# Optimization experiments

Measured on AMD Instinct MI355X. Metric: run time of the kernel, lower is better.

Reference implementation:

```python
import jax, jax.numpy as jnp
import numpy as np

NUM_HEADS = 16
LN_EPS = 1e-6

B, S, D, INTER = 16, 729, 1152, 4304


def setup_inputs() -> dict:
    key = jax.random.key(0)
    ks = jax.random.split(key, 8)
    std = 0.02
    return {
        "hidden_state": jax.random.normal(ks[0], (B, S, D), jnp.float32),
        "probe": jax.random.normal(ks[1], (1, 1, D), jnp.float32),
        "in_proj_weight": jax.random.normal(ks[2], (3 * D, D), jnp.float32) * std,
        "in_proj_bias": jax.random.normal(ks[3], (3 * D,), jnp.float32) * std,
        "ln_weight": jnp.ones((D,), jnp.float32),
        "ln_bias": jnp.zeros((D,), jnp.float32),
        "fc1_w": jax.random.normal(ks[4], (INTER, D), jnp.float32) * std,
        "fc1_b": jnp.zeros((INTER,), jnp.float32),
        "fc2_w": jax.random.normal(ks[5], (D, INTER), jnp.float32) * std,
        "fc2_b": jnp.zeros((D,), jnp.float32),
    }


def reference(hidden_state, probe, in_proj_weight, in_proj_bias,
              ln_weight, ln_bias, fc1_w, fc1_b, fc2_w, fc2_b):
    b, s, d = hidden_state.shape
    h = NUM_HEADS
    hd = d // h
    Wq, Wk, Wv = in_proj_weight[:d], in_proj_weight[d:2 * d], in_proj_weight[2 * d:]
    bq, bk, bv = in_proj_bias[:d], in_proj_bias[d:2 * d], in_proj_bias[2 * d:]

    # Projections (F.linear: x @ W.T + b)
    q = jnp.broadcast_to(probe, (b, 1, d)) @ Wq.T + bq          # [b,1,d]
    k = hidden_state @ Wk.T + bk                                 # [b,s,d]
    v = hidden_state @ Wv.T + bv                                 # [b,s,d] (this is the 'value' the head keeps)

    # Single-query attention scores per head; embed splits to (h, hd)
    qh = q.reshape(b, h, hd) / jnp.sqrt(jnp.asarray(hd, q.dtype))  # [b,h,hd]
    kh = k.reshape(b, s, h, hd)                                    # [b,s,h,hd]
    scores = jnp.einsum('bhd,bshd->bhs', qh, kh)                   # [b,h,s]
    attn_weights = jax.nn.softmax(scores, axis=-1)                 # [b,h,s]
    # NOTE: original module computes attn_output + out_proj but discards them.

    # Residual MLP on value
    mu = jnp.mean(v, axis=-1, keepdims=True)
    var = jnp.var(v, axis=-1, keepdims=True)
    vn = (v - mu) / jnp.sqrt(var + LN_EPS) * ln_weight + ln_bias
    mlp = jax.nn.gelu(vn @ fc1_w.T + fc1_b, approximate=True) @ fc2_w.T + fc2_b
    out = v + mlp                                                  # [b,s,d]
    return out, attn_weights
```

## Files before the change

### kernel.cpp

```cpp
#include <hip/hip_runtime.h>
#include <hip/hip_bf16.h>

typedef __bf16 bf16;
typedef __bf16 bf16x4 __attribute__((ext_vector_type(4)));
typedef __bf16 bf16x8 __attribute__((ext_vector_type(8)));
typedef float f32x4 __attribute__((ext_vector_type(4)));

#define NB 16
#define NS 729
#define ND 1152
#define NDP 1280
#define NH 16
#define NHD 72
#define NI 4304
#define NM (NB*NS)
#define MP 11776
#define NIP 4352
#define NQ (ND/4)
#define OUT0 ((size_t)NM*(size_t)ND)
#define LNEPS 1e-6f

#define GLOAD16(gp, lp) __builtin_amdgcn_global_load_lds( \
    (const __attribute__((address_space(1))) void*)(gp),  \
    (__attribute__((address_space(3))) void*)(lp), 16, 0, 0)

static __device__ __forceinline__ void nt_store_f32(float v, float* p) {
  __builtin_nontemporal_store(v, p);
}

__global__ __launch_bounds__(256) void k_conv_w(const float* __restrict__ src,
                                                bf16* __restrict__ dst,
                                                int sR, int sC, int dR, int dC) {
  int idx = blockIdx.x * 256 + threadIdx.x;
  int rowlen = dC >> 2;
  int r = idx / rowlen;
  int c = (idx - r * rowlen) * 4;
  if (r >= dR) return;
  bf16x4 o;
  if (r < sR && c + 4 <= sC) {
    float4 v = *(const float4*)(&src[(size_t)r * sC + c]);
    o[0] = (bf16)v.x; o[1] = (bf16)v.y; o[2] = (bf16)v.z; o[3] = (bf16)v.w;
  } else {
    o[0] = (bf16)0.f; o[1] = (bf16)0.f; o[2] = (bf16)0.f; o[3] = (bf16)0.f;
  }
  *(bf16x4*)(&dst[(size_t)r * dC + c]) = o;
}

__global__ __launch_bounds__(256) void k_q(const float* __restrict__ Wq,
                                           const float* __restrict__ probe,
                                           const float* __restrict__ bq,
                                           float* __restrict__ q) {
  int d = blockIdx.x;
  const float* wrow = Wq + (size_t)d * ND;
  float s = 0.f;
  for (int e = threadIdx.x; e < ND; e += 256) s += wrow[e] * probe[e];
  for (int o = 32; o; o >>= 1) s += __shfl_down(s, o, 64);
  __shared__ float sm[4];
  if ((threadIdx.x & 63) == 0) sm[threadIdx.x >> 6] = s;
  __syncthreads();
  if (threadIdx.x == 0) q[d] = sm[0] + sm[1] + sm[2] + sm[3] + bq[d];
}

__global__ __launch_bounds__(256) void k_qk(const float* __restrict__ Wk,
                                            const float* __restrict__ bk,
                                            const float* __restrict__ q,
                                            float* __restrict__ qk,
                                            float* __restrict__ qb) {
  int idx = blockIdx.x * 256 + threadIdx.x;
  if (idx >= NH * ND) return;
  int h = idx / ND, e = idx - h * ND;
  const float scale = 0.11785113019775793f;
  float s = 0.f;
  for (int j = 0; j < NHD; ++j)
    s += q[h * NHD + j] * Wk[(size_t)(h * NHD + j) * ND + e];
  qk[idx] = s * scale;
  if (e == 0) {
    float sb = 0.f;
    for (int j = 0; j < NHD; ++j) sb += q[h * NHD + j] * bk[h * NHD + j];
    qb[h] = sb * scale;
  }
}

__global__ __launch_bounds__(256) void k_scores(const float* __restrict__ hs,
                                                const float* __restrict__ qk,
                                                const float* __restrict__ qb,
                                                float* __restrict__ attn,
                                                bf16* __restrict__ hsb) {
  int p = blockIdx.x;
  int t = threadIdx.x;
  bf16x4* orow4 = (bf16x4*)(hsb + (size_t)p * ND);
  if (p >= NM) {
    bf16x4 z;
    z[0] = (bf16)0.f; z[1] = (bf16)0.f; z[2] = (bf16)0.f; z[3] = (bf16)0.f;
    for (int i = t; i < NQ; i += 256) orow4[i] = z;
    return;
  }
  const f32x4* row4 = (const f32x4*)(hs + (size_t)p * ND);
  const f32x4* qk4 = (const f32x4*)qk;
  float acc[NH];
#pragma unroll
  for (int h = 0; h < NH; ++h) acc[h] = 0.f;
  for (int i = t; i < NQ; i += 256) {
    f32x4 x = __builtin_nontemporal_load(&row4[i]);
    bf16x4 o;
    o[0] = (bf16)x[0]; o[1] = (bf16)x[1]; o[2] = (bf16)x[2]; o[3] = (bf16)x[3];
    orow4[i] = o;
#pragma unroll
    for (int h = 0; h < NH; ++h) {
      f32x4 wv = qk4[h * NQ + i];
      acc[h] = fmaf(x[0], wv[0],
               fmaf(x[1], wv[1], fmaf(x[2], wv[2], fmaf(x[3], wv[3], acc[h]))));
    }
  }
  __shared__ float part[NH][257];
#pragma unroll
  for (int h = 0; h < NH; ++h) part[h][t] = acc[h];
  __syncthreads();
  int h = t >> 4, l = t & 15;
  float s = 0.f;
#pragma unroll
  for (int k = 0; k < 16; ++k) s += part[h][l + k * 16];
#pragma unroll
  for (int o = 8; o; o >>= 1) s += __shfl_xor(s, o, 16);
  if (l == 0) {
    int b = p / NS, si = p - b * NS;
    attn[((size_t)(b * NH + h)) * NS + si] = s + qb[h];
  }
}

__global__ __launch_bounds__(256) void k_softmax(float* __restrict__ attn) {
  float* a = attn + (size_t)blockIdx.x * NS;
  int t = threadIdx.x;
  float x0 = (t < NS) ? a[t] : -1e30f;
  float x1 = (t + 256 < NS) ? a[t + 256] : -1e30f;
  float x2 = (t + 512 < NS) ? a[t + 512] : -1e30f;
  float mx = fmaxf(x0, fmaxf(x1, x2));
  for (int o = 32; o; o >>= 1) mx = fmaxf(mx, __shfl_down(mx, o, 64));
  __shared__ float sm[4], sm2[4];
  if ((t & 63) == 0) sm[t >> 6] = mx;
  __syncthreads();
  mx = fmaxf(fmaxf(sm[0], sm[1]), fmaxf(sm[2], sm[3]));
  float e0 = (t < NS) ? __expf(x0 - mx) : 0.f;
  float e1 = (t + 256 < NS) ? __expf(x1 - mx) : 0.f;
  float e2 = (t + 512 < NS) ? __expf(x2 - mx) : 0.f;
  float s = e0 + e1 + e2;
  for (int o = 32; o; o >>= 1) s += __shfl_down(s, o, 64);
  if ((t & 63) == 0) sm2[t >> 6] = s;
  __syncthreads();
  float inv = 1.f / (sm2[0] + sm2[1] + sm2[2] + sm2[3]);
  if (t < NS) a[t] = e0 * inv;
  if (t + 256 < NS) a[t + 256] = e1 * inv;
  if (t + 512 < NS) a[t + 512] = e2 * inv;
}

__global__ __launch_bounds__(256) void k_ln(const float* __restrict__ v,
                                            const float* __restrict__ lw,
                                            const float* __restrict__ lb,
                                            bf16* __restrict__ vn) {
  int r = blockIdx.x;
  int t = threadIdx.x;
  bf16x4* vn4 = (bf16x4*)(vn + (size_t)r * ND);
  if (r >= NM) {
    bf16x4 z;
    z[0] = (bf16)0.f; z[1] = (bf16)0.f; z[2] = (bf16)0.f; z[3] = (bf16)0.f;
    for (int i = t; i < NQ; i += 256) vn4[i] = z;
    return;
  }
  const f32x4* row4 = (const f32x4*)(v + (size_t)r * ND);
  f32x4 x0 = row4[t];
  f32x4 x1 = {0.f, 0.f, 0.f, 0.f};
  const bool has1 = (t + 256) < NQ;
  if (has1) x1 = row4[t + 256];
  float s = x0[0] + x0[1] + x0[2] + x0[3] + x1[0] + x1[1] + x1[2] + x1[3];
  float sq = x0[0] * x0[0] + x0[1] * x0[1] + x0[2] * x0[2] + x0[3] * x0[3] +
             x1[0] * x1[0] + x1[1] * x1[1] + x1[2] * x1[2] + x1[3] * x1[3];
  for (int o = 32; o; o >>= 1) {
    s += __shfl_down(s, o, 64);
    sq += __shfl_down(sq, o, 64);
  }
  __shared__ float smS[4], smQ[4];
  if ((t & 63) == 0) { smS[t >> 6] = s; smQ[t >> 6] = sq; }
  __syncthreads();
  s = smS[0] + smS[1] + smS[2] + smS[3];
  sq = smQ[0] + smQ[1] + smQ[2] + smQ[3];
  float mu = s * (1.f / ND);
  float var = sq * (1.f / ND) - mu * mu;
  float rstd = rsqrtf(var + LNEPS);
  const f32x4* lw4 = (const f32x4*)lw;
  const f32x4* lb4 = (const f32x4*)lb;
  {
    f32x4 wv = lw4[t], bv = lb4[t];
    bf16x4 o;
    o[0] = (bf16)((x0[0] - mu) * rstd * wv[0] + bv[0]);
    o[1] = (bf16)((x0[1] - mu) * rstd * wv[1] + bv[1]);
    o[2] = (bf16)((x0[2] - mu) * rstd * wv[2] + bv[2]);
    o[3] = (bf16)((x0[3] - mu) * rstd * wv[3] + bv[3]);
    vn4[t] = o;
  }
  if (has1) {
    f32x4 wv = lw4[t + 256], bv = lb4[t + 256];
    bf16x4 o;
    o[0] = (bf16)((x1[0] - mu) * rstd * wv[0] + bv[0]);
    o[1] = (bf16)((x1[1] - mu) * rstd * wv[1] + bv[1]);
    o[2] = (bf16)((x1[2] - mu) * rstd * wv[2] + bv[2]);
    o[3] = (bf16)((x1[3] - mu) * rstd * wv[3] + bv[3]);
    vn4[t + 256] = o;
  }
}

template <int MODE>
__global__ __launch_bounds__(512, 4) void gemm128(const bf16* __restrict__ A,
                                                  const bf16* __restrict__ Bm,
                                                  const float* __restrict__ bias,
                                                  const float* __restrict__ resid,
                                                  float* __restrict__ Cf,
                                                  bf16* __restrict__ Cb,
                                                  int K, int Mreal, int Nreal,
                                                  int ldc, int gx, int G) {
  __shared__ bf16 lds[3][384 * 32];
  const int tid = threadIdx.x;
  const int w = tid >> 6, lane = tid & 63;

  const int nwg = gridDim.x;
  const int orig = blockIdx.x;
  const int qq = nwg >> 3, rr = nwg & 7;
  const int xcd = orig & 7, idx0 = orig >> 3;
  const int wgid = (xcd < rr ? xcd * (qq + 1) : rr * (qq + 1) + (xcd - rr) * qq) + idx0;

  const int gy = nwg / gx;
  const int full = (gy / G) * G * gx;
  int bx, by;
  if (wgid < full) {
    int g = wgid / (G * gx), r2 = wgid - g * (G * gx);
    bx = r2 / G; by = g * G + (r2 - bx * G);
  } else {
    int r2 = wgid - full;
    int base = (gy / G) * G, rows = gy - base;
    bx = r2 / rows; by = base + (r2 - bx * rows);
  }
  const int row0 = by * 128, col0 = bx * 256;

  const int laneRow = lane >> 2;
  const int laneChunk = (lane & 3) ^ ((lane >> 3) & 3);

  auto STAGE_A = [&](int buf, int kt) {
    const bf16* gp = A + (size_t)(row0 + w * 16 + laneRow) * K + kt * 32 + laneChunk * 8;
    GLOAD16(gp, &lds[buf][(w * 16) * 32]);
  };
  auto STAGE_B = [&](int buf, int u, int kt) {
    const bf16* gp = Bm + (size_t)(col0 + u * 128 + w * 16 + laneRow) * K + kt * 32 + laneChunk * 8;
    GLOAD16(gp, &lds[buf][4096 + (u * 128 + w * 16) * 32]);
  };

  const int wm = w >> 2, wn = w & 3;
  const int fr = lane & 15, fq = lane >> 4;
  const int fsw = ((fq ^ ((fr >> 1) & 3)) << 3);
  const int arow = wm * 64 + fr;
  const int brow = wn * 64 + fr;

  f32x4 acc[4][4] = {};

  const int nk = K >> 5;
  STAGE_A(0, 0); STAGE_B(0, 0, 0); STAGE_B(0, 1, 0);
  if (nk > 1) {
    STAGE_A(1, 1); STAGE_B(1, 0, 1); STAGE_B(1, 1, 1);
    asm volatile("s_waitcnt vmcnt(3)" ::: "memory");
  } else {
    asm volatile("s_waitcnt vmcnt(0)" ::: "memory");
  }
  __builtin_amdgcn_s_barrier();

  int cur = 0;
  for (int t = 0; t < nk; ++t) {
    const bf16* As = &lds[cur][0];
    const bf16* Bs = &lds[cur][4096];
    if (t + 2 < nk) {
      int tgt = cur + 2; if (tgt >= 3) tgt -= 3;
      STAGE_A(tgt, t + 2);
      STAGE_B(tgt, 0, t + 2);
      STAGE_B(tgt, 1, t + 2);
    }
    bf16x8 bfr[4];
#pragma unroll
    for (int ni = 0; ni < 4; ++ni)
      bfr[ni] = *(const bf16x8*)(&Bs[(brow + ni * 16) * 32 + fsw]);
#pragma unroll
    for (int mi = 0; mi < 4; ++mi) {
      bf16x8 af = *(const bf16x8*)(&As[(arow + mi * 16) * 32 + fsw]);
#pragma unroll
      for (int ni = 0; ni < 4; ++ni)
        acc[mi][ni] = __builtin_amdgcn_mfma_f32_16x16x32_bf16(af, bfr[ni],
                                                              acc[mi][ni], 0, 0, 0);
    }
    if (t + 2 < nk)      { asm volatile("s_waitcnt vmcnt(3)" ::: "memory"); }
    else if (t + 1 < nk) { asm volatile("s_waitcnt vmcnt(0)" ::: "memory"); }
    __builtin_amdgcn_s_barrier();
    cur += 1; if (cur >= 3) cur -= 3;
  }

  const int rb = row0 + wm * 64, cb = col0 + wn * 64;
#pragma unroll
  for (int mi = 0; mi < 4; ++mi) {
#pragma unroll
    for (int ni = 0; ni < 4; ++ni) {
      int c = cb + ni * 16 + fr;
#pragma unroll
      for (int j = 0; j < 4; ++j) {
        int r = rb + mi * 16 + fq * 4 + j;
        float v = acc[mi][ni][j];
        if (MODE == 0) {
          if (r < Mreal && c < Nreal) nt_store_f32(v + bias[c], &Cf[(size_t)r * ldc + c]);
        } else if (MODE == 1) {
          float g = 0.f;
          if (c < Nreal) {
            float x = v + bias[c];
            float z = 1.5957691216057308f * (x + 0.044715f * x * x * x);
            g = x / (1.f + __expf(-z));
          }
          Cb[(size_t)r * ldc + c] = (bf16)g;
        } else {
          if (r < Mreal && c < Nreal)
            nt_store_f32(v + bias[c] + resid[(size_t)r * ldc + c],
                         &Cf[(size_t)r * ldc + c]);
        }
      }
    }
  }
}

extern "C" void kernel_launch(void* const* d_in, const int* in_sizes, int n_in,
                              void* d_out, int out_size, void* d_ws, size_t ws_size,
                              hipStream_t stream) {
  const float* hs    = (const float*)d_in[0];
  const float* probe = (const float*)d_in[1];
  const float* ipw   = (const float*)d_in[2];
  const float* ipb   = (const float*)d_in[3];
  const float* lw    = (const float*)d_in[4];
  const float* lb    = (const float*)d_in[5];
  const float* fc1w  = (const float*)d_in[6];
  const float* fc1b  = (const float*)d_in[7];
  const float* fc2w  = (const float*)d_in[8];
  const float* fc2b  = (const float*)d_in[9];
  float* out  = (float*)d_out;
  float* attn = out + OUT0;

  char* ws = (char*)d_ws;
  size_t off = 0;
  auto alloc = [&](size_t bytes) {
    char* p = ws + off;
    off += (bytes + 255) & ~(size_t)255;
    return p;
  };
  float* q  = (float*)alloc((size_t)ND * 4);
  float* qk = (float*)alloc((size_t)NH * ND * 4);
  float* qb = (float*)alloc((size_t)NH * 4);
  bf16* hsb = (bf16*)alloc((size_t)MP * ND * 2);
  bf16* wvb = (bf16*)alloc((size_t)NDP * ND * 2);
  bf16* f1b = (bf16*)alloc((size_t)NIP * ND * 2);
  bf16* f2b = (bf16*)alloc((size_t)NDP * NIP * 2);
  bf16* vnb = (bf16*)alloc((size_t)MP * ND * 2);
  bf16* h1b = (bf16*)alloc((size_t)MP * NIP * 2);

  k_conv_w<<<(NDP * (ND / 4) + 255) / 256, 256, 0, stream>>>(
      ipw + (size_t)2 * ND * ND, wvb, ND, ND, NDP, ND);
  k_conv_w<<<(NIP * (ND / 4) + 255) / 256, 256, 0, stream>>>(
      fc1w, f1b, NI, ND, NIP, ND);
  k_conv_w<<<(NDP * (NIP / 4) + 255) / 256, 256, 0, stream>>>(
      fc2w, f2b, ND, NI, NDP, NIP);

  k_q<<<ND, 256, 0, stream>>>(ipw, probe, ipb, q);
  k_qk<<<(NH * ND + 255) / 256, 256, 0, stream>>>(
      ipw + (size_t)ND * ND, ipb + ND, q, qk, qb);
  k_scores<<<MP, 256, 0, stream>>>(hs, qk, qb, attn, hsb);
  k_softmax<<<NB * NH, 256, 0, stream>>>(attn);

  gemm128<0><<<(MP / 128) * (NDP / 256), 512, 0, stream>>>(
      hsb, wvb, ipb + 2 * ND, nullptr, out, nullptr, ND, NM, ND, ND, NDP / 256,
      MP / 128);
  k_ln<<<MP, 256, 0, stream>>>(out, lw, lb, vnb);
  gemm128<1><<<(MP / 128) * (NIP / 256), 512, 0, stream>>>(
      vnb, f1b, fc1b, nullptr, nullptr, h1b, ND, MP, NI, NIP, NIP / 256,
      MP / 128);
  gemm128<2><<<(MP / 128) * (NDP / 256), 512, 0, stream>>>(
      h1b, f2b, fc2b, out, out, nullptr, NIP, NM, ND, ND, NDP / 256,
      MP / 128);
}
```

Baseline: 479.3 us.

## Store V projection in bf16, reuse buffers, add MFMA priority and retune grouping

The V projection now writes a bf16 intermediate instead of fp32 into the output buffer. LayerNorm and the fc2 residual read that bf16 copy, roughly halving the traffic for the V round trips. The change also raises wave priority around the MFMA loop, reuses the hidden-state bf16 buffer for the normalized activations, and changes the tile-grouping parameter G per GEMM. Holding the residual in bf16 loses precision in the output's residual term.

```diff
diff --git a/kernel.cpp b/kernel.cpp
--- a/kernel.cpp
+++ b/kernel.cpp
@@ -153,7 +153,7 @@
   if (t + 512 < NS) a[t + 512] = e2 * inv;
 }
 
-__global__ __launch_bounds__(256) void k_ln(const float* __restrict__ v,
+__global__ __launch_bounds__(256) void k_ln(const bf16* __restrict__ v,
                                             const float* __restrict__ lw,
                                             const float* __restrict__ lb,
                                             bf16* __restrict__ vn) {
@@ -166,11 +166,16 @@
     for (int i = t; i < NQ; i += 256) vn4[i] = z;
     return;
   }
-  const f32x4* row4 = (const f32x4*)(v + (size_t)r * ND);
-  f32x4 x0 = row4[t];
+  const bf16x4* row4 = (const bf16x4*)(v + (size_t)r * ND);
+  bf16x4 b0 = row4[t];
+  f32x4 x0 = {(float)b0[0], (float)b0[1], (float)b0[2], (float)b0[3]};
   f32x4 x1 = {0.f, 0.f, 0.f, 0.f};
   const bool has1 = (t + 256) < NQ;
-  if (has1) x1 = row4[t + 256];
+  if (has1) {
+    bf16x4 b1 = row4[t + 256];
+    x1[0] = (float)b1[0]; x1[1] = (float)b1[1];
+    x1[2] = (float)b1[2]; x1[3] = (float)b1[3];
+  }
   float s = x0[0] + x0[1] + x0[2] + x0[3] + x1[0] + x1[1] + x1[2] + x1[3];
   float sq = x0[0] * x0[0] + x0[1] * x0[1] + x0[2] * x0[2] + x0[3] * x0[3] +
              x1[0] * x1[0] + x1[1] * x1[1] + x1[2] * x1[2] + x1[3] * x1[3];
@@ -212,7 +217,7 @@
 __global__ __launch_bounds__(512, 4) void gemm128(const bf16* __restrict__ A,
                                                   const bf16* __restrict__ Bm,
                                                   const float* __restrict__ bias,
-                                                  const float* __restrict__ resid,
+                                                  const bf16* __restrict__ resid,
                                                   float* __restrict__ Cf,
                                                   bf16* __restrict__ Cb,
                                                   int K, int Mreal, int Nreal,
@@ -284,6 +289,7 @@
 #pragma unroll
     for (int ni = 0; ni < 4; ++ni)
       bfr[ni] = *(const bf16x8*)(&Bs[(brow + ni * 16) * 32 + fsw]);
+    __builtin_amdgcn_s_setprio(1);
 #pragma unroll
     for (int mi = 0; mi < 4; ++mi) {
       bf16x8 af = *(const bf16x8*)(&As[(arow + mi * 16) * 32 + fsw]);
@@ -292,6 +298,7 @@
         acc[mi][ni] = __builtin_amdgcn_mfma_f32_16x16x32_bf16(af, bfr[ni],
                                                               acc[mi][ni], 0, 0, 0);
     }
+    __builtin_amdgcn_s_setprio(0);
     if (t + 2 < nk)      { asm volatile("s_waitcnt vmcnt(3)" ::: "memory"); }
     else if (t + 1 < nk) { asm volatile("s_waitcnt vmcnt(0)" ::: "memory"); }
     __builtin_amdgcn_s_barrier();
@@ -309,7 +316,8 @@
         int r = rb + mi * 16 + fq * 4 + j;
         float v = acc[mi][ni][j];
         if (MODE == 0) {
-          if (r < Mreal && c < Nreal) nt_store_f32(v + bias[c], &Cf[(size_t)r * ldc + c]);
+          if (r < Mreal && c < Nreal)
+            Cb[(size_t)r * ldc + c] = (bf16)(v + bias[c]);
         } else if (MODE == 1) {
           float g = 0.f;
           if (c < Nreal) {
@@ -320,7 +328,7 @@
           Cb[(size_t)r * ldc + c] = (bf16)g;
         } else {
           if (r < Mreal && c < Nreal)
-            nt_store_f32(v + bias[c] + resid[(size_t)r * ldc + c],
+            nt_store_f32(v + bias[c] + (float)resid[(size_t)r * ldc + c],
                          &Cf[(size_t)r * ldc + c]);
         }
       }
@@ -355,11 +363,12 @@
   float* qk = (float*)alloc((size_t)NH * ND * 4);
   float* qb = (float*)alloc((size_t)NH * 4);
   bf16* hsb = (bf16*)alloc((size_t)MP * ND * 2);
+  bf16* vb  = (bf16*)alloc((size_t)MP * ND * 2);
   bf16* wvb = (bf16*)alloc((size_t)NDP * ND * 2);
   bf16* f1b = (bf16*)alloc((size_t)NIP * ND * 2);
   bf16* f2b = (bf16*)alloc((size_t)NDP * NIP * 2);
-  bf16* vnb = (bf16*)alloc((size_t)MP * ND * 2);
   bf16* h1b = (bf16*)alloc((size_t)MP * NIP * 2);
+  bf16* vnb = hsb;
 
   k_conv_w<<<(NDP * (ND / 4) + 255) / 256, 256, 0, stream>>>(
       ipw + (size_t)2 * ND * ND, wvb, ND, ND, NDP, ND);
@@ -375,13 +384,11 @@
   k_softmax<<<NB * NH, 256, 0, stream>>>(attn);
 
   gemm128<0><<<(MP / 128) * (NDP / 256), 512, 0, stream>>>(
-      hsb, wvb, ipb + 2 * ND, nullptr, out, nullptr, ND, NM, ND, ND, NDP / 256,
-      MP / 128);
-  k_ln<<<MP, 256, 0, stream>>>(out, lw, lb, vnb);
+      hsb, wvb, ipb + 2 * ND, nullptr, nullptr, vb, ND, NM, ND, ND,
+      NDP / 256, 8);
+  k_ln<<<MP, 256, 0, stream>>>(vb, lw, lb, vnb);
   gemm128<1><<<(MP / 128) * (NIP / 256), 512, 0, stream>>>(
-      vnb, f1b, fc1b, nullptr, nullptr, h1b, ND, MP, NI, NIP, NIP / 256,
-      MP / 128);
+      vnb, f1b, fc1b, nullptr, nullptr, h1b, ND, MP, NI, NIP, NIP / 256, 8);
   gemm128<2><<<(MP / 128) * (NDP / 256), 512, 0, stream>>>(
-      h1b, f2b, fc2b, out, out, nullptr, NIP, NM, ND, ND, NDP / 256,
-      MP / 128);
-}
+      h1b, f2b, fc2b, vb, out, nullptr, NIP, NM, ND, ND, NDP / 256, 2);
+}
```

New measurement: 451.1 us, median of 2. -5.9%, faster.
